# Optimization experiments

Hardware: AMD Instinct MI355X
Metric: run time of the kernel (lower is better)

The kernel has to match this reference:

```python
import jax, jax.numpy as jnp
import numpy as np

B, S, E, H = 2, 2048, 1024, 16
HD = E // H  # 64
NEG = -1e24


def setup_inputs() -> dict:
    key = jax.random.key(0)
    ks = jax.random.split(key, 20)
    sc_e = 1.0 / np.sqrt(E)
    inp = {
        "q_matrix": jax.random.normal(ks[0], (B, S, E), jnp.float32),
        "k_matrix": jax.random.normal(ks[1], (B, S, E), jnp.float32),
        "v_matrix": jax.random.normal(ks[2], (B, S, E), jnp.float32),
        "mask": jax.random.randint(ks[3], (B, S, S), 0, 2).astype(bool),
        # global QKV projections (embed_dim -> embed_dim)
        "Wq": jax.random.normal(ks[4], (E, E), jnp.float32) * sc_e,
        "bq": jnp.zeros((E,), jnp.float32),
        "Wk": jax.random.normal(ks[5], (E, E), jnp.float32) * sc_e,
        "bk": jnp.zeros((E,), jnp.float32),
        "Wv": jax.random.normal(ks[6], (E, E), jnp.float32) * sc_e,
        "bv": jnp.zeros((E,), jnp.float32),
        # per-head QKV projections (embed_dim -> head_dim), batched over heads
        "Whq": jax.random.normal(ks[7], (H, E, HD), jnp.float32) * sc_e,
        "bhq": jnp.zeros((H, HD), jnp.float32),
        "Whk": jax.random.normal(ks[8], (H, E, HD), jnp.float32) * sc_e,
        "bhk": jnp.zeros((H, HD), jnp.float32),
        "Whv": jax.random.normal(ks[9], (H, E, HD), jnp.float32) * sc_e,
        "bhv": jnp.zeros((H, HD), jnp.float32),
        # output projection
        "Wo": jax.random.normal(ks[10], (E, E), jnp.float32) * sc_e,
        "bo": jnp.zeros((E,), jnp.float32),
    }
    return inp


def reference(q_matrix, k_matrix, v_matrix, mask, Wq, bq, Wk, bk, Wv, bv,
              Whq, bhq, Whk, bhk, Whv, bhv, Wo, bo):
    # global projections [B,S,E]
    qg = q_matrix @ Wq + bq
    kg = k_matrix @ Wk + bk
    vg = v_matrix @ Wv + bv
    # per-head projections -> [B,H,S,HD]
    qh = jnp.einsum('bse,hed->bhsd', qg, Whq) + bhq[None, :, None, :]
    kh = jnp.einsum('bse,hed->bhsd', kg, Whk) + bhk[None, :, None, :]
    vh = jnp.einsum('bse,hed->bhsd', vg, Whv) + bhv[None, :, None, :]
    # scaled dot-product attention, scores [B,H,S,S]
    scores = jnp.einsum('bhsd,bhtd->bhst', qh, kh) / jnp.sqrt(jnp.float32(HD))
    scores = jnp.where(mask[:, None, :, :], NEG, scores)
    weights = jax.nn.softmax(scores, axis=-1)
    out = jnp.einsum('bhst,bhtd->bhsd', weights, vh)
    # concat heads (head order along last dim, matching torch.cat)
    x = out.transpose(0, 2, 1, 3).reshape(out.shape[0], out.shape[2], E)
    return x @ Wo + bo
```

## Files before the change

kernel.cpp:

```cpp
#include <hip/hip_runtime.h>
#include <hip/hip_bf16.h>

typedef unsigned short us16;
typedef __attribute__((ext_vector_type(8))) short short8;
typedef __attribute__((ext_vector_type(4))) float float4v;

#define E_DIM 1024
#define S_LEN 2048
#define B_DIM 2
#define H_DIM 16
#define HD_DIM 64
#define M_ROWS 4096
#define SCALE2 0.18033688011112042f

__device__ __forceinline__ float b2f(us16 b) {
    return __uint_as_float(((unsigned int)b) << 16);
}
__device__ __forceinline__ us16 f2b(float f) {
    unsigned int u = __float_as_uint(f);
    unsigned int r = (u + 0x7fffu + ((u >> 16) & 1u)) >> 16;
    return (us16)r;
}
__device__ __forceinline__ unsigned pack2(float a, float b) {
    return ((__float_as_uint(a) + 0x8000u) >> 16) |
           ((__float_as_uint(b) + 0x8000u) & 0xFFFF0000u);
}

__device__ __forceinline__ void gload16(const us16* g, us16* lds_uniform_base) {
    __builtin_amdgcn_global_load_lds(
        (const __attribute__((address_space(1))) void*)g,
        (__attribute__((address_space(3))) void*)lds_uniform_base, 16, 0, 0);
}

__global__ __launch_bounds__(256) void prep(
    const float* __restrict__ q, const float* __restrict__ k, const float* __restrict__ v,
    const float* __restrict__ Wq, const float* __restrict__ Wk, const float* __restrict__ Wv,
    const float* __restrict__ Whq, const float* __restrict__ Whk, const float* __restrict__ Whv,
    const float* __restrict__ Wo,
    const float* __restrict__ bq, const float* __restrict__ bk, const float* __restrict__ bv,
    const float* __restrict__ bhq, const float* __restrict__ bhk, const float* __restrict__ bhv,
    const int* __restrict__ mask,
    us16* qb, us16* kb, us16* vb, us16* Wqb, us16* Wkb, us16* Wvb,
    us16* WhqT, us16* WhkT, us16* WhvT, us16* WoT,
    unsigned long long* mbits,
    float* bcq, float* bck, float* bcv, float* zbias)
{
    __shared__ us16 tile[32][33];
    __shared__ float red[4][64];
    int blk = blockIdx.x, tid = threadIdx.x;

    if (blk < 7680) {
        const float* in; us16* out; int idx;
        if (blk < 6144) {
            int z = blk >> 11, rem = blk & 2047;
            in = z == 0 ? q : z == 1 ? k : v;
            out = z == 0 ? qb : z == 1 ? kb : vb;
            idx = (rem * 256 + tid) * 8;
        } else {
            int t = blk - 6144, z = t >> 9, rem = t & 511;
            in = z == 0 ? Wq : z == 1 ? Wk : Wv;
            out = z == 0 ? Wqb : z == 1 ? Wkb : Wvb;
            idx = (rem * 256 + tid) * 8;
        }
        float4 f0 = *(const float4*)(in + idx);
        float4 f1 = *(const float4*)(in + idx + 4);
        us16 t8[8] = {f2b(f0.x), f2b(f0.y), f2b(f0.z), f2b(f0.w),
                      f2b(f1.x), f2b(f1.y), f2b(f1.z), f2b(f1.w)};
        *(uint4*)(out + idx) = *(const uint4*)t8;
    } else if (blk < 11776) {
        int t = blk - 7680, z = t >> 10, rem = t & 1023;
        const float* in = z == 0 ? Whq : z == 1 ? Whk : z == 2 ? Whv : Wo;
        us16* out = z == 0 ? WhqT : z == 1 ? WhkT : z == 2 ? WhvT : WoT;
        int mode = (z < 3) ? 1 : 0;
        int bx = rem & 31, by = rem >> 5;
        int tx = tid & 31, ty = tid >> 5;
#pragma unroll
        for (int i = 0; i < 4; ++i) {
            int e = by * 32 + ty + i * 8;
            int c = bx * 32 + tx;
            size_t src;
            if (mode == 0) src = (size_t)e * E_DIM + c;
            else           src = ((size_t)(c >> 6) * E_DIM + e) * 64 + (c & 63);
            tile[ty + i * 8][tx] = f2b(in[src]);
        }
        __syncthreads();
#pragma unroll
        for (int i = 0; i < 4; ++i) {
            int c = bx * 32 + ty + i * 8;
            int e = by * 32 + tx;
            out[(size_t)c * E_DIM + e] = tile[tx][ty + i * 8];
        }
    } else if (blk < 12800) {
        int row = (blk - 11776) * 4 + (tid >> 6);
        int lane = tid & 63;
        const int* mp = mask + (size_t)row * S_LEN;
        for (int w = 0; w < 32; ++w) {
            int mv = mp[w * 64 + lane];
            unsigned long long bal = __ballot(mv != 0);
            if (lane == 0) mbits[(size_t)row * 32 + w] = bal;
        }
    } else if (blk < 12848) {
        int t = blk - 12800, z = t >> 4, h = t & 15;
        const float* bg = z == 0 ? bq : z == 1 ? bk : bv;
        const float* Wh = z == 0 ? Whq : z == 1 ? Whk : Whv;
        const float* bh = z == 0 ? bhq : z == 1 ? bhk : bhv;
        float* bc = z == 0 ? bcq : z == 1 ? bck : bcv;
        float sc = (z == 0) ? SCALE2 : 1.0f;
        int d = tid & 63, part = tid >> 6;
        float acc = 0.f;
        int j0 = part * 256;
        for (int j = j0; j < j0 + 256; ++j)
            acc += bg[j] * Wh[((size_t)h * E_DIM + j) * HD_DIM + d];
        red[part][d] = acc;
        __syncthreads();
        if (tid < 64)
            bc[h * 64 + tid] = (red[0][tid] + red[1][tid] + red[2][tid] + red[3][tid] + bh[h * 64 + tid]) * sc;
    } else {
        int i = (blk - 12848) * 256 + tid;
        if (i < 1024) zbias[i] = 0.f;
    }
}

#define BK 32

__device__ __forceinline__ void gemm_body(
    const us16* __restrict__ A, const us16* __restrict__ Bt,
    const float* __restrict__ bias, void* __restrict__ Cp,
    int M, int N, int K, int bxt, int byt, int omode)
{
    __shared__ us16 As[128 * BK];
    __shared__ us16 Bs[128 * BK];

    int tid = threadIdx.x;
    int wave = tid >> 6, lane = tid & 63;
    int quad = lane >> 4, l16 = lane & 15;
    int wm = (wave >> 1) * 64, wn = (wave & 1) * 64;
    int bm0 = byt * 128, bn0 = bxt * 128;
    int srow = lane >> 2;
    int gcol = (((lane & 3) ^ (srow & 3)) << 3);
    int rslot = ((quad ^ (l16 & 3)) << 3);

    float4v acc[4][4];
#pragma unroll
    for (int i = 0; i < 4; ++i)
#pragma unroll
        for (int j = 0; j < 4; ++j)
#pragma unroll
            for (int r = 0; r < 4; ++r) acc[i][j][r] = 0.f;

    for (int k0 = 0; k0 < K; k0 += BK) {
#pragma unroll
        for (int c = 0; c < 2; ++c) {
            int r0 = 32 * wave + 16 * c;
            gload16(A  + (size_t)(bm0 + r0 + srow) * K + k0 + gcol, &As[r0 * BK]);
            gload16(Bt + (size_t)(bn0 + r0 + srow) * K + k0 + gcol, &Bs[r0 * BK]);
        }
        __syncthreads();
        short8 af[4], bfr[4];
#pragma unroll
        for (int i = 0; i < 4; ++i)
            af[i] = *(const short8*)&As[(wm + i * 16 + l16) * BK + rslot];
#pragma unroll
        for (int j = 0; j < 4; ++j)
            bfr[j] = *(const short8*)&Bs[(wn + j * 16 + l16) * BK + rslot];
#pragma unroll
        for (int i = 0; i < 4; ++i)
#pragma unroll
            for (int j = 0; j < 4; ++j)
                acc[i][j] = __builtin_amdgcn_mfma_f32_16x16x32_bf16(af[i], bfr[j], acc[i][j], 0, 0, 0);
        __syncthreads();
    }

#pragma unroll
    for (int i = 0; i < 4; ++i) {
#pragma unroll
        for (int j = 0; j < 4; ++j) {
#pragma unroll
            for (int r = 0; r < 4; ++r) {
                int row = bm0 + wm + i * 16 + quad * 4 + r;
                int col = bn0 + wn + j * 16 + l16;
                float vv = acc[i][j][r] + ((omode == 3) ? bias[row] : bias[col]);
                if (omode == 1) {
                    int b = row >> 11, s = row & 2047, h = col >> 6, d = col & 63;
                    ((us16*)Cp)[(((size_t)(b * H_DIM + h) * S_LEN + s) * HD_DIM) + d] = f2b(vv);
                } else {
                    int h = row >> 6, d = row & 63, b = col >> 11, sl = col & 2047;
                    ((us16*)Cp)[(((size_t)(b * H_DIM + h) * HD_DIM + d) * S_LEN) + sl] = f2b(vv);
                }
            }
        }
    }
}

__global__ __launch_bounds__(256) void proj_all(
    const us16* __restrict__ qb, const us16* __restrict__ kb, const us16* __restrict__ vb,
    const us16* __restrict__ WcqT, const us16* __restrict__ WckT, const us16* __restrict__ WcvT,
    const float* __restrict__ bcq, const float* __restrict__ bck, const float* __restrict__ bcv,
    us16* __restrict__ qhb, us16* __restrict__ khb, us16* __restrict__ vtb)
{
    int bx = blockIdx.x;
    int z = bx >> 8, t = bx & 255;
    if (z == 0)      gemm_body(qb, WcqT, bcq, qhb, M_ROWS, E_DIM, E_DIM, t & 7, t >> 3, 1);
    else if (z == 1) gemm_body(kb, WckT, bck, khb, M_ROWS, E_DIM, E_DIM, t & 7, t >> 3, 1);
    else             gemm_body(WcvT, vb, bcv, vtb, E_DIM, M_ROWS, E_DIM, t & 31, t >> 5, 3);
}

template<int OMODE>
__device__ __forceinline__ void gemm64_body(
    const us16* __restrict__ A, const us16* __restrict__ Bt,
    const float* __restrict__ bias, void* __restrict__ Cp,
    int M, int N, int K, int bxt, int byt, float oscale)
{
    __shared__ us16 As[64 * BK];
    __shared__ us16 Bs[128 * BK];

    int tid = threadIdx.x;
    int wave = tid >> 6, lane = tid & 63;
    int quad = lane >> 4, l16 = lane & 15;
    int wm = (wave >> 1) * 32, wn = (wave & 1) * 64;
    int bm0 = byt * 64, bn0 = bxt * 128;
    int srow = lane >> 2;
    int gcol = (((lane & 3) ^ (srow & 3)) << 3);
    int rslot = ((quad ^ (l16 & 3)) << 3);

    float4v acc[2][4];
#pragma unroll
    for (int i = 0; i < 2; ++i)
#pragma unroll
        for (int j = 0; j < 4; ++j)
#pragma unroll
            for (int r = 0; r < 4; ++r) acc[i][j][r] = 0.f;

    for (int k0 = 0; k0 < K; k0 += BK) {
        gload16(A + (size_t)(bm0 + 16 * wave + srow) * K + k0 + gcol, &As[16 * wave * BK]);
#pragma unroll
        for (int c = 0; c < 2; ++c) {
            int r0 = 32 * wave + 16 * c;
            gload16(Bt + (size_t)(bn0 + r0 + srow) * K + k0 + gcol, &Bs[r0 * BK]);
        }
        __syncthreads();
        short8 af[2], bfr[4];
#pragma unroll
        for (int i = 0; i < 2; ++i)
            af[i] = *(const short8*)&As[(wm + i * 16 + l16) * BK + rslot];
#pragma unroll
        for (int j = 0; j < 4; ++j)
            bfr[j] = *(const short8*)&Bs[(wn + j * 16 + l16) * BK + rslot];
#pragma unroll
        for (int i = 0; i < 2; ++i)
#pragma unroll
            for (int j = 0; j < 4; ++j)
                acc[i][j] = __builtin_amdgcn_mfma_f32_16x16x32_bf16(af[i], bfr[j], acc[i][j], 0, 0, 0);
        __syncthreads();
    }

#pragma unroll
    for (int i = 0; i < 2; ++i)
#pragma unroll
        for (int j = 0; j < 4; ++j)
#pragma unroll
            for (int r = 0; r < 4; ++r) {
                int row = bm0 + wm + i * 16 + quad * 4 + r;
                int col = bn0 + wn + j * 16 + l16;
                float vv = (acc[i][j][r] + bias[col]) * oscale;
                if (OMODE == 0) ((us16*)Cp)[(size_t)row * N + col] = f2b(vv);
                else            ((float*)Cp)[(size_t)row * N + col] = vv;
            }
}

__global__ __launch_bounds__(256) void wgemm3(
    const us16* A0, const us16* A1, const us16* A2,
    const us16* B0, const us16* B1, const us16* B2,
    const float* zbias, us16* C0, us16* C1, us16* C2)
{
    int z = blockIdx.z;
    const us16* A = z == 0 ? A0 : z == 1 ? A1 : A2;
    const us16* Bt = z == 0 ? B0 : z == 1 ? B1 : B2;
    us16* C = z == 0 ? C0 : z == 1 ? C1 : C2;
    float sc = (z == 0) ? SCALE2 : 1.0f;
    gemm64_body<0>(A, Bt, zbias, C, E_DIM, E_DIM, E_DIM, blockIdx.x, blockIdx.y, sc);
}

__global__ __launch_bounds__(256) void gemm_out64(
    const us16* __restrict__ A, const us16* __restrict__ Bt,
    const float* __restrict__ bias, float* __restrict__ C, int M, int N, int K)
{
    gemm64_body<2>(A, Bt, bias, C, M, N, K, blockIdx.x, blockIdx.y, 1.0f);
}

#define PST 72

__global__ __launch_bounds__(512) void attn_kernel(
    const us16* __restrict__ qh, const us16* __restrict__ kh,
    const us16* __restrict__ vt, const unsigned long long* __restrict__ mbits,
    us16* __restrict__ o_p, float* __restrict__ l_p)
{
    __shared__ us16 Ks[64 * 64];
    __shared__ us16 Vs[64 * 64];
    __shared__ us16 Pw[8][16 * PST];

    int tid = threadIdx.x;
    int w = tid >> 6, lane = tid & 63;
    int quad = lane >> 4, l16 = lane & 15;
    int bh = blockIdx.y;
    int b = bh >> 4;
    int z = blockIdx.z;
    int q0 = blockIdx.x * 128;
    const size_t base = (size_t)bh * (S_LEN * HD_DIM);

    int qrow = q0 + w * 16 + l16;
    short8 qf0, qf1;
    {
        const us16* qp = qh + base + (size_t)qrow * HD_DIM + quad * 8;
        qf0 = *(const short8*)qp;
        qf1 = *(const short8*)(qp + 32);
    }

    int strow = w * 8 + (lane >> 3);
    int scol = ((lane & 7) ^ (strow & 7)) * 8;
    us16* kdst = &Ks[w * 512];
    us16* vdst = &Vs[w * 512];
    const us16* ksrc0 = kh + base + (size_t)strow * HD_DIM + scol;
    const us16* vsrc0 = vt + base + (size_t)strow * S_LEN + scol;

    int slotA = (quad ^ (l16 & 7)) * 8;
    int slotB = ((quad ^ (l16 & 7)) ^ 4) * 8;

    float lsum = 0.f;
    float4v o[4];
#pragma unroll
    for (int dt = 0; dt < 4; ++dt)
#pragma unroll
        for (int r = 0; r < 4; ++r) o[dt][r] = 0.f;

    const unsigned long long* mrow = mbits + ((size_t)(b * S_LEN + qrow) * 32) + z * 16;

    for (int kt = z * 1024; kt < z * 1024 + 1024; kt += 64) {
        __syncthreads();
        gload16(ksrc0 + (size_t)kt * HD_DIM, kdst);
        gload16(vsrc0 + kt, vdst);
        __syncthreads();

        unsigned long long mw = *mrow++;

        float4v sc[4];
#pragma unroll
        for (int ct = 0; ct < 4; ++ct) {
            int t = ct * 16 + l16;
            short8 kf0 = *(const short8*)&Ks[t * 64 + slotA];
            short8 kf1 = *(const short8*)&Ks[t * 64 + slotB];
            float4v a;
#pragma unroll
            for (int r = 0; r < 4; ++r) a[r] = 0.f;
            a = __builtin_amdgcn_mfma_f32_16x16x32_bf16(kf0, qf0, a, 0, 0, 0);
            a = __builtin_amdgcn_mfma_f32_16x16x32_bf16(kf1, qf1, a, 0, 0, 0);
            sc[ct] = a;
        }

#pragma unroll
        for (int ct = 0; ct < 4; ++ct) {
            unsigned bits = (unsigned)(mw >> (ct * 16 + quad * 4));
            float p[4];
#pragma unroll
            for (int r = 0; r < 4; ++r) {
                float pin = ((bits >> r) & 1u) ? -1e38f : sc[ct][r];
                p[r] = __builtin_amdgcn_exp2f(pin);
                lsum += p[r];
            }
            uint2 pk;
            pk.x = pack2(p[0], p[1]);
            pk.y = pack2(p[2], p[3]);
            *(uint2*)&Pw[w][l16 * PST + ct * 16 + quad * 4] = pk;
        }

        short8 pf0 = *(const short8*)&Pw[w][l16 * PST + quad * 8];
        short8 pf1 = *(const short8*)&Pw[w][l16 * PST + 32 + quad * 8];
#pragma unroll
        for (int dt = 0; dt < 4; ++dt) {
            int d = dt * 16 + l16;
            short8 vf0 = *(const short8*)&Vs[d * 64 + slotA];
            short8 vf1 = *(const short8*)&Vs[d * 64 + slotB];
            o[dt] = __builtin_amdgcn_mfma_f32_16x16x32_bf16(pf0, vf0, o[dt], 0, 0, 0);
            o[dt] = __builtin_amdgcn_mfma_f32_16x16x32_bf16(pf1, vf1, o[dt], 0, 0, 0);
        }
    }

    lsum += __shfl_xor(lsum, 16, 64);
    lsum += __shfl_xor(lsum, 32, 64);
    if (lane < 16)
        l_p[(size_t)z * 65536 + bh * S_LEN + qrow] = lsum;

    int rowg = bh * S_LEN + q0 + w * 16 + quad * 4;
#pragma unroll
    for (int dt = 0; dt < 4; ++dt)
#pragma unroll
        for (int r = 0; r < 4; ++r)
            o_p[(size_t)z * 4194304 + (size_t)(rowg + r) * 64 + dt * 16 + l16] = f2b(o[dt][r]);
}

__global__ __launch_bounds__(256) void attn_combine(
    const us16* __restrict__ o_p, const float* __restrict__ l_p,
    us16* __restrict__ x)
{
    int fidx = blockIdx.x * 256 + threadIdx.x;
    int rix = fidx >> 3;
    int d8 = (fidx & 7) * 8;
    float linv = 1.0f / (l_p[rix] + l_p[65536 + rix]);
    uint4 a = *(const uint4*)(o_p + (size_t)rix * 64 + d8);
    uint4 c = *(const uint4*)(o_p + 4194304 + (size_t)rix * 64 + d8);
    const us16* ap = (const us16*)&a;
    const us16* cp = (const us16*)&c;
    us16 t8[8];
#pragma unroll
    for (int i = 0; i < 8; ++i)
        t8[i] = f2b((b2f(ap[i]) + b2f(cp[i])) * linv);
    int bh = rix >> 11, b = bh >> 4, h = bh & 15, s = rix & 2047;
    *(uint4*)&x[(size_t)(b * S_LEN + s) * E_DIM + h * HD_DIM + d8] = *(const uint4*)t8;
}

extern "C" void kernel_launch(void* const* d_in, const int* in_sizes, int n_in,
                              void* d_out, int out_size, void* d_ws, size_t ws_size,
                              hipStream_t stream) {
    const float* q    = (const float*)d_in[0];
    const float* k    = (const float*)d_in[1];
    const float* v    = (const float*)d_in[2];
    const int*   mask = (const int*)d_in[3];
    const float* Wq = (const float*)d_in[4];   const float* bq = (const float*)d_in[5];
    const float* Wk = (const float*)d_in[6];   const float* bk = (const float*)d_in[7];
    const float* Wv = (const float*)d_in[8];   const float* bv = (const float*)d_in[9];
    const float* Whq = (const float*)d_in[10]; const float* bhq = (const float*)d_in[11];
    const float* Whk = (const float*)d_in[12]; const float* bhk = (const float*)d_in[13];
    const float* Whv = (const float*)d_in[14]; const float* bhv = (const float*)d_in[15];
    const float* Wo = (const float*)d_in[16];  const float* bo = (const float*)d_in[17];

    us16* ws = (us16*)d_ws;
    const size_t M1 = (size_t)1 << 20;
    us16* WhqT = ws + 0 * M1;
    us16* WhkT = ws + 1 * M1;
    us16* WhvT = ws + 2 * M1;
    us16* WoT  = ws + 3 * M1;
    us16* WcqT = ws + 4 * M1;
    us16* WckT = ws + 5 * M1;
    us16* WcvT = ws + 6 * M1;
    us16* Wqb  = ws + 7 * M1;
    us16* Wkb  = ws + 8 * M1;
    us16* Wvb  = ws + 9 * M1;
    us16* qb   = ws + 10 * M1;
    us16* kb   = ws + 14 * M1;
    us16* vb   = ws + 18 * M1;
    us16* qhb  = ws + 22 * M1;
    us16* khb  = ws + 26 * M1;
    us16* vtb  = ws + 30 * M1;
    us16* o_p  = qb;
    us16* xb   = vb;
    float* bcq   = (float*)(ws + 34 * M1);
    float* bck   = bcq + 1024;
    float* bcv   = bck + 1024;
    float* zbias = bcv + 1024;
    unsigned long long* mbits = (unsigned long long*)(ws + 34 * M1 + 16384);
    float* l_p = (float*)(ws + 34 * M1 + 16384 + 524288);

    prep<<<12852, 256, 0, stream>>>(q, k, v, Wq, Wk, Wv, Whq, Whk, Whv, Wo,
                                    bq, bk, bv, bhq, bhk, bhv, mask,
                                    qb, kb, vb, Wqb, Wkb, Wvb,
                                    WhqT, WhkT, WhvT, WoT, mbits,
                                    bcq, bck, bcv, zbias);

    wgemm3<<<dim3(8, 16, 3), 256, 0, stream>>>(WhqT, WhkT, WhvT, Wqb, Wkb, Wvb, zbias,
                                               WcqT, WckT, WcvT);

    proj_all<<<768, 256, 0, stream>>>(qb, kb, vb, WcqT, WckT, WcvT,
                                      bcq, bck, bcv, qhb, khb, vtb);

    attn_kernel<<<dim3(16, 32, 2), 512, 0, stream>>>(qhb, khb, vtb, mbits, o_p, l_p);
    attn_combine<<<2048, 256, 0, stream>>>(o_p, l_p, xb);

    gemm_out64<<<dim3(8, 64), 256, 0, stream>>>(xb, WoT, bo, (float*)d_out,
                                                M_ROWS, E_DIM, E_DIM);
}
```

Measured before the change: 323.4 us.

## Double-buffer K/V tiles in attention with XCD-aware block mapping and MFMA priority

The attention kernel now keeps two shared-memory K/V buffers and prefetches the next 64-key tile (and its mask word) while the current tile is computed, replacing two barriers per iteration with a single waitcnt-and-barrier. The launch is flattened to a 1D grid and remapped so that blocks sharing the same batch-head land on the same XCD, aiming for better L2 reuse of K/V. MFMA sections are wrapped in s_setprio to favour matrix issue. The cost is doubled LDS for K/V, which may reduce occupancy.

```diff
diff --git a/kernel.cpp b/kernel.cpp
--- a/kernel.cpp
+++ b/kernel.cpp
@@ -289,23 +289,28 @@
 }
 
 #define PST 72
+#define NT 16
 
 __global__ __launch_bounds__(512) void attn_kernel(
     const us16* __restrict__ qh, const us16* __restrict__ kh,
     const us16* __restrict__ vt, const unsigned long long* __restrict__ mbits,
     us16* __restrict__ o_p, float* __restrict__ l_p)
 {
-    __shared__ us16 Ks[64 * 64];
-    __shared__ us16 Vs[64 * 64];
+    __shared__ us16 Ks[2][64 * 64];
+    __shared__ us16 Vs[2][64 * 64];
     __shared__ us16 Pw[8][16 * PST];
 
     int tid = threadIdx.x;
     int w = tid >> 6, lane = tid & 63;
     int quad = lane >> 4, l16 = lane & 15;
-    int bh = blockIdx.y;
+
+    int wg = blockIdx.x;
+    int xcd = wg & 7, idx = wg >> 3;
+    int bh = xcd * 4 + (idx >> 5);
+    int rem = idx & 31;
+    int z = rem >> 4;
+    int q0 = (rem & 15) * 128;
     int b = bh >> 4;
-    int z = blockIdx.z;
-    int q0 = blockIdx.x * 128;
     const size_t base = (size_t)bh * (S_LEN * HD_DIM);
 
     int qrow = q0 + w * 16 + l16;
@@ -318,13 +323,11 @@
 
     int strow = w * 8 + (lane >> 3);
     int scol = ((lane & 7) ^ (strow & 7)) * 8;
-    us16* kdst = &Ks[w * 512];
-    us16* vdst = &Vs[w * 512];
-    const us16* ksrc0 = kh + base + (size_t)strow * HD_DIM + scol;
-    const us16* vsrc0 = vt + base + (size_t)strow * S_LEN + scol;
+    const us16* ksrc0 = kh + base + ((size_t)(z * 1024 + strow)) * HD_DIM + scol;
+    const us16* vsrc0 = vt + base + (size_t)strow * S_LEN + scol + z * 1024;
 
     int slotA = (quad ^ (l16 & 7)) * 8;
-    int slotB = ((quad ^ (l16 & 7)) ^ 4) * 8;
+    int slotB = slotA ^ 32;
 
     float lsum = 0.f;
     float4v o[4];
@@ -335,20 +338,32 @@
 
     const unsigned long long* mrow = mbits + ((size_t)(b * S_LEN + qrow) * 32) + z * 16;
 
-    for (int kt = z * 1024; kt < z * 1024 + 1024; kt += 64) {
-        __syncthreads();
-        gload16(ksrc0 + (size_t)kt * HD_DIM, kdst);
-        gload16(vsrc0 + kt, vdst);
-        __syncthreads();
-
-        unsigned long long mw = *mrow++;
+    gload16(ksrc0, &Ks[0][w * 512]);
+    gload16(vsrc0, &Vs[0][w * 512]);
+    unsigned long long mw = mrow[0];
+    asm volatile("s_waitcnt vmcnt(0)" ::: "memory");
+    __builtin_amdgcn_s_barrier();
+    __builtin_amdgcn_sched_barrier(0);
+
+    for (int t = 0; t < NT; ++t) {
+        int cur = t & 1;
+        const us16* KsC = Ks[cur];
+        const us16* VsC = Vs[cur];
+
+        unsigned long long mwn = 0ull;
+        if (t + 1 < NT) {
+            gload16(ksrc0 + (size_t)((t + 1) * 64) * HD_DIM, &Ks[cur ^ 1][w * 512]);
+            gload16(vsrc0 + (t + 1) * 64, &Vs[cur ^ 1][w * 512]);
+            mwn = mrow[t + 1];
+        }
 
         float4v sc[4];
+        __builtin_amdgcn_s_setprio(1);
 #pragma unroll
         for (int ct = 0; ct < 4; ++ct) {
-            int t = ct * 16 + l16;
-            short8 kf0 = *(const short8*)&Ks[t * 64 + slotA];
-            short8 kf1 = *(const short8*)&Ks[t * 64 + slotB];
+            int tt = ct * 16 + l16;
+            short8 kf0 = *(const short8*)&KsC[tt * 64 + slotA];
+            short8 kf1 = *(const short8*)&KsC[tt * 64 + slotB];
             float4v a;
 #pragma unroll
             for (int r = 0; r < 4; ++r) a[r] = 0.f;
@@ -356,6 +371,7 @@
             a = __builtin_amdgcn_mfma_f32_16x16x32_bf16(kf1, qf1, a, 0, 0, 0);
             sc[ct] = a;
         }
+        __builtin_amdgcn_s_setprio(0);
 
 #pragma unroll
         for (int ct = 0; ct < 4; ++ct) {
@@ -375,14 +391,21 @@
 
         short8 pf0 = *(const short8*)&Pw[w][l16 * PST + quad * 8];
         short8 pf1 = *(const short8*)&Pw[w][l16 * PST + 32 + quad * 8];
+        __builtin_amdgcn_s_setprio(1);
 #pragma unroll
         for (int dt = 0; dt < 4; ++dt) {
             int d = dt * 16 + l16;
-            short8 vf0 = *(const short8*)&Vs[d * 64 + slotA];
-            short8 vf1 = *(const short8*)&Vs[d * 64 + slotB];
+            short8 vf0 = *(const short8*)&VsC[d * 64 + slotA];
+            short8 vf1 = *(const short8*)&VsC[d * 64 + slotB];
             o[dt] = __builtin_amdgcn_mfma_f32_16x16x32_bf16(pf0, vf0, o[dt], 0, 0, 0);
             o[dt] = __builtin_amdgcn_mfma_f32_16x16x32_bf16(pf1, vf1, o[dt], 0, 0, 0);
         }
+        __builtin_amdgcn_s_setprio(0);
+
+        mw = mwn;
+        asm volatile("s_waitcnt vmcnt(0)" ::: "memory");
+        __builtin_amdgcn_s_barrier();
+        __builtin_amdgcn_sched_barrier(0);
     }
 
     lsum += __shfl_xor(lsum, 16, 64);
@@ -472,7 +495,7 @@
     proj_all<<<768, 256, 0, stream>>>(qb, kb, vb, WcqT, WckT, WcvT,
                                       bcq, bck, bcv, qhb, khb, vtb);
 
-    attn_kernel<<<dim3(16, 32, 2), 512, 0, stream>>>(qhb, khb, vtb, mbits, o_p, l_p);
+    attn_kernel<<<1024, 512, 0, stream>>>(qhb, khb, vtb, mbits, o_p, l_p);
     attn_combine<<<2048, 256, 0, stream>>>(o_p, l_p, xb);
 
     gemm_out64<<<dim3(8, 64), 256, 0, stream>>>(xb, WoT, bo, (float*)d_out,
```

Measured after the change: 319.9 us. Within noise of the previous version (-1.1%).
